# Optimization experiments

Measured on AMD Instinct MI355X. Metric: run time of the kernel, lower is better.

Reference implementation:

```python
import jax, jax.numpy as jnp
import numpy as np

B, C, H, W = 8, 384, 32, 32
NUM_HEADS = 8
HEAD_DIM = C // NUM_HEADS


def setup_inputs() -> dict:
    key = jax.random.key(0)
    k1, k2, k3, k4, k5 = jax.random.split(key, 5)
    s = 1.0 / np.sqrt(C)
    return {
        "x": jax.random.normal(k1, (B, C, H, W), dtype=jnp.float32),
        "w_qkv": jax.random.normal(k2, (3 * C, C), dtype=jnp.float32) * s,   # 1x1 conv == linear over channels
        "b_qkv": jax.random.normal(k3, (3 * C,), dtype=jnp.float32) * 0.01,
        "w_proj": jax.random.normal(k4, (C, C), dtype=jnp.float32) * s,
        "b_proj": jax.random.normal(k5, (C,), dtype=jnp.float32) * 0.01,
    }


def reference(x, w_qkv, b_qkv, w_proj, b_proj):
    b, c, h, w = x.shape
    n = h * w
    scale = HEAD_DIM ** (-0.5)
    # 1x1 conv qkv: (B, 3C, H, W)
    qkv = jnp.einsum('bchw,oc->bohw', x, w_qkv) + b_qkv[None, :, None, None]
    # 'b (three hd d) h0 w0 -> three b hd (h0 w0) d'
    qkv = qkv.reshape(b, 3, NUM_HEADS, HEAD_DIM, n)
    qkv = jnp.transpose(qkv, (1, 0, 2, 4, 3))  # (3, B, heads, N, d)
    q, k, v = qkv[0], qkv[1], qkv[2]
    attn = jnp.einsum('bhnd,bhmd->bhnm', q, k) * scale
    attn = jax.nn.softmax(attn, axis=-1)
    out = jnp.einsum('bhnm,bhmd->bhnd', attn, v)          # (B, heads, N, d)
    out = jnp.transpose(out, (0, 1, 3, 2)).reshape(b, c, h, w)  # b (hd d) h w
    out = jnp.einsum('bchw,oc->bohw', out, w_proj) + b_proj[None, :, None, None]
    return out
```

## Files before the change

### kernel.cpp

```cpp
#include <hip/hip_runtime.h>
#include <hip/hip_bf16.h>

typedef __hip_bfloat16 bf16;
typedef __bf16 bfx8 __attribute__((ext_vector_type(8)));
typedef float f32x4 __attribute__((ext_vector_type(4)));

#define Bk   8
#define Ck   384
#define NHk  8
#define Dk   48
#define Dp   64
#define Nk   1024
#define O3   1152


__global__ __launch_bounds__(256) void padzero_kernel(
    bf16* __restrict__ Qp, bf16* __restrict__ Kp)
{
    int idx = blockIdx.x * 256 + threadIdx.x;
    int buf  = idx >> 17;
    int row  = (idx >> 1) & 65535;
    int half = idx & 1;
    bf16* p = (buf ? Kp : Qp) + (size_t)row * Dp + 48 + half * 8;
    *(int4*)p = (int4){0, 0, 0, 0};
}

__global__ __launch_bounds__(256) void xpose_kernel(
    const float* __restrict__ x, bf16* __restrict__ Xs)
{
    __shared__ bf16 tile[32][33];
    const int b = blockIdx.z, c0 = blockIdx.y * 32, n0 = blockIdx.x * 32;
    const int tn = threadIdx.x & 31, tc = threadIdx.x >> 5;
    const float* xb = x + (size_t)b * Ck * Nk;
    #pragma unroll
    for (int i = 0; i < 4; ++i)
        tile[tc + 8 * i][tn] = __float2bfloat16(xb[(size_t)(c0 + tc + 8 * i) * Nk + n0 + tn]);
    __syncthreads();
    bf16* base = Xs + ((size_t)b * 64 + (n0 >> 4)) * 48 * 128 + (c0 >> 3) * 128;
    #pragma unroll
    for (int i = 0; i < 4; ++i) {
        int n_loc = tc + 8 * i, c_loc = tn;
        base[(size_t)(n_loc >> 4) * 6144 + (c_loc >> 3) * 128 +
             (n_loc & 15) * 8 + (c_loc & 7)] = tile[c_loc][n_loc];
    }
}

__global__ __launch_bounds__(256) void wconv_kernel(
    const float* __restrict__ wq, const float* __restrict__ wp,
    bf16* __restrict__ Wq, bf16* __restrict__ Wp)
{
    int i = blockIdx.x * 256 + threadIdx.x;
    if (i < O3 * Ck) {
        int o = i / Ck, c = i - o * Ck;
        Wq[((size_t)(o >> 4) * 48 + (c >> 3)) * 128 + (o & 15) * 8 + (c & 7)] =
            __float2bfloat16(wq[i]);
    }
    if (i < Ck * Ck) {
        int o = i / Ck, c = i - o * Ck;
        Wp[((size_t)(o >> 4) * 48 + (c >> 3)) * 128 + (o & 15) * 8 + (c & 7)] =
            __float2bfloat16(wp[i]);
    }
}

__global__ __launch_bounds__(256) void qkv_mfma_kernel(
    const bf16* __restrict__ Xs, const bf16* __restrict__ Wq,
    const float* __restrict__ bias,
    bf16* __restrict__ Qp, bf16* __restrict__ Kp, bf16* __restrict__ Vt)
{
    const int b    = blockIdx.z;
    const int by   = blockIdx.y;
    const int bx   = blockIdx.x;
    const int o0   = by * 64;
    const int n0   = bx * 128;
    const int wave = threadIdx.x >> 6;
    const int lane = threadIdx.x & 63;
    const int l15  = lane & 15, quad = lane >> 4;
    const int t3   = o0 / Ck;

    const bf16* xg[2];
    const bf16* wg[4];
    #pragma unroll
    for (int i = 0; i < 2; ++i)
        xg[i] = Xs + ((size_t)(b * 64 + bx * 8 + wave * 2 + i) * 48) * 128 + lane * 8;
    #pragma unroll
    for (int j = 0; j < 4; ++j)
        wg[j] = Wq + ((size_t)(by * 4 + j) * 48) * 128 + lane * 8;

    f32x4 acc[8];
    #pragma unroll
    for (int i = 0; i < 8; ++i) acc[i] = (f32x4){0.f, 0.f, 0.f, 0.f};

    if (t3 < 2) {
        #pragma unroll
        for (int s = 0; s < 12; ++s) {
            bfx8 fx[2], fw[4];
            #pragma unroll
            for (int i = 0; i < 2; ++i) fx[i] = *(const bfx8*)(xg[i] + s * 512);
            #pragma unroll
            for (int j = 0; j < 4; ++j) fw[j] = *(const bfx8*)(wg[j] + s * 512);
            #pragma unroll
            for (int i = 0; i < 2; ++i)
                #pragma unroll
                for (int j = 0; j < 4; ++j)
                    acc[i * 4 + j] = __builtin_amdgcn_mfma_f32_16x16x32_bf16(
                        fx[i], fw[j], acc[i * 4 + j], 0, 0, 0);
        }
        const float qscale = 0.144337567297406441f;
        #pragma unroll
        for (int j = 0; j < 4; ++j) {
            int o  = o0 + j * 16 + l15;
            float bi = bias[o];
            int r  = o - t3 * Ck;
            int hd = r / Dk, d = r - hd * Dk;
            bf16* dst = (t3 == 0 ? Qp : Kp) + ((size_t)(b * NHk + hd) * Nk) * Dp + d;
            #pragma unroll
            for (int i = 0; i < 2; ++i) {
                #pragma unroll
                for (int reg = 0; reg < 4; ++reg) {
                    int npos = n0 + wave * 32 + i * 16 + quad * 4 + reg;
                    float v = acc[i * 4 + j][reg] + bi;
                    if (t3 == 0) v *= qscale;
                    dst[(size_t)npos * Dp] = __float2bfloat16(v);
                }
            }
        }
    } else {
        #pragma unroll
        for (int s = 0; s < 12; ++s) {
            bfx8 fx[2], fw[4];
            #pragma unroll
            for (int i = 0; i < 2; ++i) fx[i] = *(const bfx8*)(xg[i] + s * 512);
            #pragma unroll
            for (int j = 0; j < 4; ++j) fw[j] = *(const bfx8*)(wg[j] + s * 512);
            #pragma unroll
            for (int j = 0; j < 4; ++j)
                #pragma unroll
                for (int i = 0; i < 2; ++i)
                    acc[j * 2 + i] = __builtin_amdgcn_mfma_f32_16x16x32_bf16(
                        fw[j], fx[i], acc[j * 2 + i], 0, 0, 0);
        }
        #pragma unroll
        for (int j = 0; j < 4; ++j) {
            #pragma unroll
            for (int reg = 0; reg < 4; ++reg) {
                int o  = o0 + j * 16 + quad * 4 + reg;
                float bi = bias[o];
                int r  = o - 2 * Ck;
                int hd = r / Dk, d = r - hd * Dk;
                #pragma unroll
                for (int i = 0; i < 2; ++i) {
                    int npos = n0 + wave * 32 + i * 16 + l15;
                    Vt[((size_t)(b * NHk + hd) * Dk + d) * Nk + npos] =
                        __float2bfloat16(acc[j * 2 + i][reg] + bi);
                }
            }
        }
    }
}

__global__ __launch_bounds__(256) void attn_kernel(
    const bf16* __restrict__ Qp, const bf16* __restrict__ Kp,
    const bf16* __restrict__ Vt, bf16* __restrict__ AO)
{
    __shared__ __align__(16) short Ks[64 * 72];
    __shared__ __align__(16) short Vs[48 * 72];
    __shared__ __align__(16) short Ps[4 * 32 * 72];
    __shared__ float sums[4][32];

    const int bx   = blockIdx.x;
    const int n0   = bx * 128;
    const int hd   = blockIdx.y;
    const int b    = blockIdx.z;
    const int t    = threadIdx.x;
    const int wave = t >> 6;
    const int lane = t & 63;
    const int l15  = lane & 15;
    const int quad = lane >> 4;

    const bf16* qb = Qp + (size_t)(b * NHk + hd) * Nk * Dp;
    const bf16* kb = Kp + (size_t)(b * NHk + hd) * Nk * Dp;
    const bf16* vb = Vt + (size_t)(b * NHk + hd) * Dk * Nk;

    bfx8 bq[2][2];
    #pragma unroll
    for (int g = 0; g < 2; ++g) {
        const bf16* qr = qb + (size_t)(n0 + wave * 32 + g * 16 + l15) * Dp;
        bq[g][0] = *(const bfx8*)(qr + quad * 8);
        bq[g][1] = *(const bfx8*)(qr + 32 + quad * 8);
    }

    float l_run[2] = {0.f, 0.f};
    f32x4 oacc[2][3];
    #pragma unroll
    for (int g = 0; g < 2; ++g)
        #pragma unroll
        for (int dc = 0; dc < 3; ++dc) oacc[g][dc] = (f32x4){0.f, 0.f, 0.f, 0.f};

    short* PsW = Ps + wave * 32 * 72;

    for (int k0 = 0; k0 < Nk; k0 += 64) {
        __syncthreads();
        {
            const bf16* src = kb + (size_t)k0 * Dp;
            #pragma unroll
            for (int i = 0; i < 2; ++i) {
                int c = t + 256 * i;
                int row = c >> 3, part = c & 7;
                *(bfx8*)&Ks[row * 72 + part * 8] = *(const bfx8*)(src + c * 8);
            }
            for (int c = t; c < 384; c += 256) {
                int d = c >> 3, part = c & 7;
                *(bfx8*)&Vs[d * 72 + part * 8] =
                    *(const bfx8*)(vb + (size_t)d * Nk + k0 + part * 8);
            }
        }
        __syncthreads();

        f32x4 sf[4][2];
        #pragma unroll
        for (int s = 0; s < 4; ++s) {
            const bfx8 kf0 = *(const bfx8*)&Ks[(s * 16 + l15) * 72 + quad * 8];
            const bfx8 kf1 = *(const bfx8*)&Ks[(s * 16 + l15) * 72 + 32 + quad * 8];
            #pragma unroll
            for (int g = 0; g < 2; ++g) {
                f32x4 z = (f32x4){0.f, 0.f, 0.f, 0.f};
                z = __builtin_amdgcn_mfma_f32_16x16x32_bf16(kf0, bq[g][0], z, 0, 0, 0);
                z = __builtin_amdgcn_mfma_f32_16x16x32_bf16(kf1, bq[g][1], z, 0, 0, 0);
                sf[s][g] = z;
            }
        }

        #pragma unroll
        for (int g = 0; g < 2; ++g) {
            float lsum = 0.f;
            #pragma unroll
            for (int s = 0; s < 4; ++s) {
                ushort4 pk;
                float e0 = __expf(sf[s][g][0]);
                float e1 = __expf(sf[s][g][1]);
                float e2 = __expf(sf[s][g][2]);
                float e3 = __expf(sf[s][g][3]);
                lsum += (e0 + e1) + (e2 + e3);
                bf16 h0 = __float2bfloat16(e0), h1 = __float2bfloat16(e1);
                bf16 h2 = __float2bfloat16(e2), h3 = __float2bfloat16(e3);
                pk.x = *(unsigned short*)&h0; pk.y = *(unsigned short*)&h1;
                pk.z = *(unsigned short*)&h2; pk.w = *(unsigned short*)&h3;
                *(ushort4*)&PsW[(g * 16 + l15) * 72 + s * 16 + quad * 4] = pk;
            }
            l_run[g] += lsum;
        }

        asm volatile("s_waitcnt lgkmcnt(0)" ::: "memory");

        bfx8 ap[2][2];
        #pragma unroll
        for (int g = 0; g < 2; ++g) {
            ap[g][0] = *(const bfx8*)&PsW[(g * 16 + l15) * 72 + quad * 8];
            ap[g][1] = *(const bfx8*)&PsW[(g * 16 + l15) * 72 + 32 + quad * 8];
        }
        #pragma unroll
        for (int dc = 0; dc < 3; ++dc) {
            const bfx8 bv0 = *(const bfx8*)&Vs[(dc * 16 + l15) * 72 + quad * 8];
            const bfx8 bv1 = *(const bfx8*)&Vs[(dc * 16 + l15) * 72 + 32 + quad * 8];
            #pragma unroll
            for (int g = 0; g < 2; ++g) {
                oacc[g][dc] = __builtin_amdgcn_mfma_f32_16x16x32_bf16(ap[g][0], bv0, oacc[g][dc], 0, 0, 0);
                oacc[g][dc] = __builtin_amdgcn_mfma_f32_16x16x32_bf16(ap[g][1], bv1, oacc[g][dc], 0, 0, 0);
            }
        }
    }

    #pragma unroll
    for (int g = 0; g < 2; ++g) {
        float lt = l_run[g];
        lt += __shfl_xor(lt, 16, 64);
        lt += __shfl_xor(lt, 32, 64);
        sums[wave][g * 16 + l15] = lt;
    }
    asm volatile("s_waitcnt lgkmcnt(0)" ::: "memory");

    short* OsW = PsW;
    #pragma unroll
    for (int g = 0; g < 2; ++g) {
        #pragma unroll
        for (int r = 0; r < 4; ++r) {
            int qi = g * 16 + quad * 4 + r;
            float rli = 1.0f / sums[wave][qi];
            #pragma unroll
            for (int dcc = 0; dcc < 3; ++dcc) {
                bf16 hb = __float2bfloat16(oacc[g][dcc][r] * rli);
                OsW[qi * 64 + dcc * 16 + l15] = *(short*)&hb;
            }
        }
    }
    asm volatile("s_waitcnt lgkmcnt(0)" ::: "memory");

    #pragma unroll
    for (int g = 0; g < 2; ++g) {
        bf16* aob = AO + (((size_t)b * 64 + bx * 8 + wave * 2 + g) * 48 + hd * 6) * 128;
        int u = lane;
        int4 v = *(const int4*)&OsW[(g * 16 + (u & 15)) * 64 + (u >> 4) * 8];
        *(int4*)(aob + u * 8) = v;
        if (lane < 32) {
            int u2 = 64 + lane;
            int4 v2 = *(const int4*)&OsW[(g * 16 + (u2 & 15)) * 64 + (u2 >> 4) * 8];
            *(int4*)(aob + u2 * 8) = v2;
        }
    }
}

__global__ __launch_bounds__(256) void proj_mfma_kernel(
    const bf16* __restrict__ AO, const bf16* __restrict__ Wp,
    const float* __restrict__ bias, float* __restrict__ out)
{
    const int b    = blockIdx.z;
    const int by   = blockIdx.y;
    const int bx   = blockIdx.x;
    const int o0   = by * 64;
    const int n0   = bx * 128;
    const int wave = threadIdx.x >> 6;
    const int lane = threadIdx.x & 63;
    const int l15  = lane & 15, quad = lane >> 4;

    const bf16* ag[2];
    const bf16* wg[4];
    #pragma unroll
    for (int i = 0; i < 2; ++i)
        ag[i] = AO + ((size_t)(b * 64 + bx * 8 + wave * 2 + i) * 48) * 128 + lane * 8;
    #pragma unroll
    for (int j = 0; j < 4; ++j)
        wg[j] = Wp + ((size_t)(by * 4 + j) * 48) * 128 + lane * 8;

    f32x4 acc[8];
    #pragma unroll
    for (int i = 0; i < 8; ++i) acc[i] = (f32x4){0.f, 0.f, 0.f, 0.f};

    #pragma unroll
    for (int s = 0; s < 12; ++s) {
        bfx8 fx[2], fw[4];
        #pragma unroll
        for (int i = 0; i < 2; ++i) fx[i] = *(const bfx8*)(ag[i] + s * 512);
        #pragma unroll
        for (int j = 0; j < 4; ++j) fw[j] = *(const bfx8*)(wg[j] + s * 512);
        #pragma unroll
        for (int j = 0; j < 4; ++j)
            #pragma unroll
            for (int i = 0; i < 2; ++i)
                acc[j * 2 + i] = __builtin_amdgcn_mfma_f32_16x16x32_bf16(
                    fw[j], fx[i], acc[j * 2 + i], 0, 0, 0);
    }

    #pragma unroll
    for (int j = 0; j < 4; ++j) {
        #pragma unroll
        for (int reg = 0; reg < 4; ++reg) {
            int o  = o0 + j * 16 + quad * 4 + reg;
            float bi = bias[o];
            #pragma unroll
            for (int i = 0; i < 2; ++i) {
                int npos = n0 + wave * 32 + i * 16 + l15;
                out[((size_t)b * Ck + o) * Nk + npos] = acc[j * 2 + i][reg] + bi;
            }
        }
    }
}

extern "C" void kernel_launch(void* const* d_in, const int* in_sizes, int n_in,
                              void* d_out, int out_size, void* d_ws, size_t ws_size,
                              hipStream_t stream)
{
    const float* x      = (const float*)d_in[0];
    const float* w_qkv  = (const float*)d_in[1];
    const float* b_qkv  = (const float*)d_in[2];
    const float* w_proj = (const float*)d_in[3];
    const float* b_proj = (const float*)d_in[4];
    float* out = (float*)d_out;

    const size_t XT_SEG = (size_t)Bk * Nk * Ck;
    const size_t WQ_SEG = (size_t)O3 * Ck;
    const size_t WP_SEG = (size_t)Ck * Ck;
    const size_t QK_SEG = (size_t)Bk * NHk * Nk * Dp;
    const size_t V_SEG  = (size_t)Bk * NHk * Dk * Nk;

    bf16* Xs = (bf16*)d_ws;
    bf16* Wq = Xs + XT_SEG;
    bf16* Wp = Wq + WQ_SEG;
    bf16* Qp = Wp + WP_SEG;
    bf16* Kp = Qp + QK_SEG;
    bf16* Vt = Kp + QK_SEG;
    bf16* AO = Vt + V_SEG;

    padzero_kernel<<<1024, 256, 0, stream>>>(Qp, Kp);
    xpose_kernel<<<dim3(Nk / 32, Ck / 32, Bk), 256, 0, stream>>>(x, Xs);
    wconv_kernel<<<(O3 * Ck + 255) / 256, 256, 0, stream>>>(w_qkv, w_proj, Wq, Wp);
    qkv_mfma_kernel<<<dim3(Nk / 128, O3 / 64, Bk), 256, 0, stream>>>(
        Xs, Wq, b_qkv, Qp, Kp, Vt);
    attn_kernel<<<dim3(Nk / 128, NHk, Bk), 256, 0, stream>>>(Qp, Kp, Vt, AO);
    proj_mfma_kernel<<<dim3(Nk / 128, Ck / 64, Bk), 256, 0, stream>>>(
        AO, Wp, b_proj, out);
}
```

Baseline: 139.6 us.

## Store Q/K/V in MFMA fragment layout and read attention operands directly from global

The QKV projection now writes Q, K and V in a pre-swizzled 16x8 fragment layout, so the attention kernel can load MFMA operands straight from global/L2 with one 16-byte load per lane. This drops the per-tile LDS staging of K and V and both block-wide barriers in the key loop. The padding-zero kernel is folded into the weight conversion kernel to save a launch, and the softmax uses exp2 with log2(e) folded into the Q scale. In exchange, K/V reuse across the four waves now depends on cache hits instead of shared memory, which adds global load latency to each iteration.

Result: slower. 146.0 us (+4.6%).

```diff
diff --git a/kernel.cpp b/kernel.cpp
--- a/kernel.cpp
+++ b/kernel.cpp
@@ -14,17 +14,6 @@
 #define O3   1152
 
 
-__global__ __launch_bounds__(256) void padzero_kernel(
-    bf16* __restrict__ Qp, bf16* __restrict__ Kp)
-{
-    int idx = blockIdx.x * 256 + threadIdx.x;
-    int buf  = idx >> 17;
-    int row  = (idx >> 1) & 65535;
-    int half = idx & 1;
-    bf16* p = (buf ? Kp : Qp) + (size_t)row * Dp + 48 + half * 8;
-    *(int4*)p = (int4){0, 0, 0, 0};
-}
-
 __global__ __launch_bounds__(256) void xpose_kernel(
     const float* __restrict__ x, bf16* __restrict__ Xs)
 {
@@ -47,7 +36,8 @@
 
 __global__ __launch_bounds__(256) void wconv_kernel(
     const float* __restrict__ wq, const float* __restrict__ wp,
-    bf16* __restrict__ Wq, bf16* __restrict__ Wp)
+    bf16* __restrict__ Wq, bf16* __restrict__ Wp,
+    bf16* __restrict__ Qs, bf16* __restrict__ Ks)
 {
     int i = blockIdx.x * 256 + threadIdx.x;
     if (i < O3 * Ck) {
@@ -60,12 +50,23 @@
         Wp[((size_t)(o >> 4) * 48 + (c >> 3)) * 128 + (o & 15) * 8 + (c & 7)] =
             __float2bfloat16(wp[i]);
     }
+    if (i < 262144) {
+        int buf = i >> 17;
+        int r17 = i & 131071;
+        int head = r17 >> 11;
+        int r11 = r17 & 2047;
+        int g = r11 >> 5, c5 = r11 & 31;
+        int cd = 6 + (c5 >> 4), e = c5 & 15;
+        bf16* p = (buf ? Ks : Qs) + (size_t)head * 65536 +
+                  ((size_t)g * 8 + cd) * 128 + e * 8;
+        *(int4*)p = (int4){0, 0, 0, 0};
+    }
 }
 
 __global__ __launch_bounds__(256) void qkv_mfma_kernel(
     const bf16* __restrict__ Xs, const bf16* __restrict__ Wq,
     const float* __restrict__ bias,
-    bf16* __restrict__ Qp, bf16* __restrict__ Kp, bf16* __restrict__ Vt)
+    bf16* __restrict__ Qs, bf16* __restrict__ Ks, bf16* __restrict__ Vs)
 {
     const int b    = blockIdx.z;
     const int by   = blockIdx.y;
@@ -105,14 +106,15 @@
                     acc[i * 4 + j] = __builtin_amdgcn_mfma_f32_16x16x32_bf16(
                         fx[i], fw[j], acc[i * 4 + j], 0, 0, 0);
         }
-        const float qscale = 0.144337567297406441f;
+        const float qscale = 0.2082350964f;
         #pragma unroll
         for (int j = 0; j < 4; ++j) {
             int o  = o0 + j * 16 + l15;
             float bi = bias[o];
             int r  = o - t3 * Ck;
             int hd = r / Dk, d = r - hd * Dk;
-            bf16* dst = (t3 == 0 ? Qp : Kp) + ((size_t)(b * NHk + hd) * Nk) * Dp + d;
+            bf16* hb = (t3 == 0 ? Qs : Ks) + (size_t)(b * NHk + hd) * 65536
+                     + (d >> 3) * 128 + (d & 7);
             #pragma unroll
             for (int i = 0; i < 2; ++i) {
                 #pragma unroll
@@ -120,7 +122,7 @@
                     int npos = n0 + wave * 32 + i * 16 + quad * 4 + reg;
                     float v = acc[i * 4 + j][reg] + bi;
                     if (t3 == 0) v *= qscale;
-                    dst[(size_t)npos * Dp] = __float2bfloat16(v);
+                    hb[(size_t)(npos >> 4) * 1024 + (npos & 15) * 8] = __float2bfloat16(v);
                 }
             }
         }
@@ -147,10 +149,12 @@
                 float bi = bias[o];
                 int r  = o - 2 * Ck;
                 int hd = r / Dk, d = r - hd * Dk;
+                bf16* vb = Vs + (size_t)(b * NHk + hd) * 49152
+                         + ((size_t)(d >> 4) * 128) * 128 + (d & 15) * 8;
                 #pragma unroll
                 for (int i = 0; i < 2; ++i) {
                     int npos = n0 + wave * 32 + i * 16 + l15;
-                    Vt[((size_t)(b * NHk + hd) * Dk + d) * Nk + npos] =
+                    vb[(size_t)(npos >> 3) * 128 + (npos & 7)] =
                         __float2bfloat16(acc[j * 2 + i][reg] + bi);
                 }
             }
@@ -159,16 +163,13 @@
 }
 
 __global__ __launch_bounds__(256) void attn_kernel(
-    const bf16* __restrict__ Qp, const bf16* __restrict__ Kp,
-    const bf16* __restrict__ Vt, bf16* __restrict__ AO)
-{
-    __shared__ __align__(16) short Ks[64 * 72];
-    __shared__ __align__(16) short Vs[48 * 72];
+    const bf16* __restrict__ Qs, const bf16* __restrict__ Ks,
+    const bf16* __restrict__ Vs, bf16* __restrict__ AO)
+{
     __shared__ __align__(16) short Ps[4 * 32 * 72];
     __shared__ float sums[4][32];
 
     const int bx   = blockIdx.x;
-    const int n0   = bx * 128;
     const int hd   = blockIdx.y;
     const int b    = blockIdx.z;
     const int t    = threadIdx.x;
@@ -177,16 +178,16 @@
     const int l15  = lane & 15;
     const int quad = lane >> 4;
 
-    const bf16* qb = Qp + (size_t)(b * NHk + hd) * Nk * Dp;
-    const bf16* kb = Kp + (size_t)(b * NHk + hd) * Nk * Dp;
-    const bf16* vb = Vt + (size_t)(b * NHk + hd) * Dk * Nk;
+    const bf16* qb = Qs + (size_t)(b * NHk + hd) * 65536;
+    const bf16* kb = Ks + (size_t)(b * NHk + hd) * 65536;
+    const bf16* vb = Vs + (size_t)(b * NHk + hd) * 49152;
 
     bfx8 bq[2][2];
     #pragma unroll
     for (int g = 0; g < 2; ++g) {
-        const bf16* qr = qb + (size_t)(n0 + wave * 32 + g * 16 + l15) * Dp;
-        bq[g][0] = *(const bfx8*)(qr + quad * 8);
-        bq[g][1] = *(const bfx8*)(qr + 32 + quad * 8);
+        const bf16* qp = qb + ((size_t)(bx * 8 + wave * 2 + g) * 8 + quad) * 128 + l15 * 8;
+        bq[g][0] = *(const bfx8*)(qp);
+        bq[g][1] = *(const bfx8*)(qp + 512);
     }
 
     float l_run[2] = {0.f, 0.f};
@@ -199,28 +200,12 @@
     short* PsW = Ps + wave * 32 * 72;
 
     for (int k0 = 0; k0 < Nk; k0 += 64) {
-        __syncthreads();
-        {
-            const bf16* src = kb + (size_t)k0 * Dp;
-            #pragma unroll
-            for (int i = 0; i < 2; ++i) {
-                int c = t + 256 * i;
-                int row = c >> 3, part = c & 7;
-                *(bfx8*)&Ks[row * 72 + part * 8] = *(const bfx8*)(src + c * 8);
-            }
-            for (int c = t; c < 384; c += 256) {
-                int d = c >> 3, part = c & 7;
-                *(bfx8*)&Vs[d * 72 + part * 8] =
-                    *(const bfx8*)(vb + (size_t)d * Nk + k0 + part * 8);
-            }
-        }
-        __syncthreads();
-
         f32x4 sf[4][2];
         #pragma unroll
         for (int s = 0; s < 4; ++s) {
-            const bfx8 kf0 = *(const bfx8*)&Ks[(s * 16 + l15) * 72 + quad * 8];
-            const bfx8 kf1 = *(const bfx8*)&Ks[(s * 16 + l15) * 72 + 32 + quad * 8];
+            const bf16* kp = kb + ((size_t)((k0 >> 4) + s) * 8 + quad) * 128 + l15 * 8;
+            const bfx8 kf0 = *(const bfx8*)(kp);
+            const bfx8 kf1 = *(const bfx8*)(kp + 512);
             #pragma unroll
             for (int g = 0; g < 2; ++g) {
                 f32x4 z = (f32x4){0.f, 0.f, 0.f, 0.f};
@@ -236,10 +221,10 @@
             #pragma unroll
             for (int s = 0; s < 4; ++s) {
                 ushort4 pk;
-                float e0 = __expf(sf[s][g][0]);
-                float e1 = __expf(sf[s][g][1]);
-                float e2 = __expf(sf[s][g][2]);
-                float e3 = __expf(sf[s][g][3]);
+                float e0 = __builtin_amdgcn_exp2f(sf[s][g][0]);
+                float e1 = __builtin_amdgcn_exp2f(sf[s][g][1]);
+                float e2 = __builtin_amdgcn_exp2f(sf[s][g][2]);
+                float e3 = __builtin_amdgcn_exp2f(sf[s][g][3]);
                 lsum += (e0 + e1) + (e2 + e3);
                 bf16 h0 = __float2bfloat16(e0), h1 = __float2bfloat16(e1);
                 bf16 h2 = __float2bfloat16(e2), h3 = __float2bfloat16(e3);
@@ -260,8 +245,9 @@
         }
         #pragma unroll
         for (int dc = 0; dc < 3; ++dc) {
-            const bfx8 bv0 = *(const bfx8*)&Vs[(dc * 16 + l15) * 72 + quad * 8];
-            const bfx8 bv1 = *(const bfx8*)&Vs[(dc * 16 + l15) * 72 + 32 + quad * 8];
+            const bf16* vp = vb + ((size_t)dc * 128 + (k0 >> 3) + quad) * 128 + l15 * 8;
+            const bfx8 bv0 = *(const bfx8*)(vp);
+            const bfx8 bv1 = *(const bfx8*)(vp + 512);
             #pragma unroll
             for (int g = 0; g < 2; ++g) {
                 oacc[g][dc] = __builtin_amdgcn_mfma_f32_16x16x32_bf16(ap[g][0], bv0, oacc[g][dc], 0, 0, 0);
@@ -385,17 +371,17 @@
     bf16* Xs = (bf16*)d_ws;
     bf16* Wq = Xs + XT_SEG;
     bf16* Wp = Wq + WQ_SEG;
-    bf16* Qp = Wp + WP_SEG;
-    bf16* Kp = Qp + QK_SEG;
-    bf16* Vt = Kp + QK_SEG;
-    bf16* AO = Vt + V_SEG;
-
-    padzero_kernel<<<1024, 256, 0, stream>>>(Qp, Kp);
+    bf16* Qs = Wp + WP_SEG;
+    bf16* Ks = Qs + QK_SEG;
+    bf16* Vs = Ks + QK_SEG;
+    bf16* AO = Vs + V_SEG;
+
     xpose_kernel<<<dim3(Nk / 32, Ck / 32, Bk), 256, 0, stream>>>(x, Xs);
-    wconv_kernel<<<(O3 * Ck + 255) / 256, 256, 0, stream>>>(w_qkv, w_proj, Wq, Wp);
+    wconv_kernel<<<(O3 * Ck + 255) / 256, 256, 0, stream>>>(
+        w_qkv, w_proj, Wq, Wp, Qs, Ks);
     qkv_mfma_kernel<<<dim3(Nk / 128, O3 / 64, Bk), 256, 0, stream>>>(
-        Xs, Wq, b_qkv, Qp, Kp, Vt);
-    attn_kernel<<<dim3(Nk / 128, NHk, Bk), 256, 0, stream>>>(Qp, Kp, Vt, AO);
+        Xs, Wq, b_qkv, Qs, Ks, Vs);
+    attn_kernel<<<dim3(Nk / 128, NHk, Bk), 256, 0, stream>>>(Qs, Ks, Vs, AO);
     proj_mfma_kernel<<<dim3(Nk / 128, Ck / 64, Bk), 256, 0, stream>>>(
         AO, Wp, b_proj, out);
 }
```
